# Performance work log

Hardware: AMD Instinct MI355X
Metric: run time of the kernel (lower is better)

Reference implementation:

```python
import jax, jax.numpy as jnp
import numpy as np

N_NODE, N_REL = 200000, 64
DIM, N_FACTOR, N_LAYER, K, B = 64, 4, 2, 32, 1024


def setup_inputs() -> dict:
    key = jax.random.key(0)
    ks = jax.random.split(key, 12)
    node_emb = jax.random.normal(ks[0], (N_NODE, N_FACTOR, DIM), jnp.float32) * 0.05
    relation_emb = jax.random.normal(ks[1], (N_REL, N_FACTOR, DIM), jnp.float32) * 0.05
    # attention MLP: Linear(2d -> d), ReLU, Linear(d -> 1); stored as [in, out]
    W1 = jax.random.normal(ks[2], (2 * DIM, DIM), jnp.float32) * (1.0 / np.sqrt(2 * DIM))
    b1 = jnp.zeros((DIM,), jnp.float32)
    W2 = jax.random.normal(ks[3], (DIM, 1), jnp.float32) * (1.0 / np.sqrt(DIM))
    b2 = jnp.zeros((1,), jnp.float32)
    users = jax.random.randint(ks[4], (B,), 0, N_NODE)
    items = jax.random.randint(ks[5], (B,), 0, N_NODE)

    def make_triple(kh, kr, kt):
        h = jax.random.randint(kh, (B, 1, N_LAYER, K), 0, N_NODE)
        r = jax.random.randint(kr, (B, 1, N_LAYER, K), 0, N_REL)
        t = jax.random.randint(kt, (B, 1, N_LAYER, K), 0, N_NODE)
        return jnp.concatenate([h, r, t], axis=1)  # [B, 3, L, K]

    users_triple = make_triple(ks[6], ks[7], ks[8])
    items_triple = make_triple(ks[9], ks[10], ks[11])
    return {
        "node_emb": node_emb, "relation_emb": relation_emb,
        "W1": W1, "b1": b1, "W2": W2, "b2": b2,
        "users": users, "items": items,
        "users_triple": users_triple, "items_triple": items_triple,
    }


def _knowledge_attention(h_emb, t_emb, W1, b1, W2, b2):
    # h_emb, t_emb: [B, L, K, F, d]
    x = jnp.concatenate([h_emb, t_emb], axis=-1)          # [B,L,K,F,2d]
    hid = jax.nn.relu(x @ W1 + b1)                        # [B,L,K,F,d]
    logits = jnp.squeeze(hid @ W2 + b2, axis=-1)          # [B,L,K,F]
    w = jax.nn.softmax(logits, axis=2)                    # softmax over neighbors K
    return jnp.sum(w[..., None] * t_emb, axis=2)          # [B,L,F,d]


def _tower(node_emb, idx, triple, W1, b1, W2, b2):
    origin = node_emb[idx]                                # [B,F,d]
    h = node_emb[triple[:, 0]]                            # [B,L,K,F,d]
    t = node_emb[triple[:, 2]]                            # [B,L,K,F,d]
    layers = _knowledge_attention(h, t, W1, b1, W2, b2)   # [B,L,F,d]
    emb = jnp.concatenate([origin[:, None], layers], axis=1)  # [B,L+1,F,d]
    return jnp.transpose(emb, (1, 0, 2, 3))               # [L+1,B,F,d]


def reference(node_emb, relation_emb, W1, b1, W2, b2, users, items, users_triple, items_triple):
    # relation_emb is gathered in the original but never used by the attention math.
    u = _tower(node_emb, users, users_triple, W1, b1, W2, b2)
    v = _tower(node_emb, items, items_triple, W1, b1, W2, b2)
    return jnp.stack([u, v])  # [2, L+1, B, F, d]
```

## Files before the change

### kernel.cpp

```cpp
#include <hip/hip_runtime.h>
#include <math.h>

#define NNODE  200000
#define DIM    64
#define NF     4
#define NLAYER 2
#define KK     32
#define BB     1024

typedef __bf16 bf16x8 __attribute__((ext_vector_type(8)));
typedef float  f32x4  __attribute__((ext_vector_type(4)));

__global__ void prep_w1t(const float* __restrict__ W1, __bf16* __restrict__ w1t) {
    int j = blockIdx.x * 256 + threadIdx.x;
    int d = j >> 7, i = j & 127;
    w1t[j] = (__bf16)W1[i * 64 + d];
}

__global__ __launch_bounds__(256, 3) void kgat_direct(
    const float* __restrict__ node_emb,
    const __bf16* __restrict__ w1t,
    const float* __restrict__ b1,
    const float* __restrict__ W2,
    const int*   __restrict__ users,
    const int*   __restrict__ items,
    const int*   __restrict__ users_triple,
    const int*   __restrict__ items_triple,
    float*       __restrict__ out)
{
    __shared__ float logitS[128];

    const int bid   = blockIdx.x;
    const int tower = bid >> 11;
    const int b     = (bid >> 1) & 1023;
    const int layer = bid & 1;
    const int tid   = threadIdx.x;
    const int w     = tid >> 6;
    const int lane  = tid & 63;
    const int m16   = lane & 15;
    const int quad  = lane >> 4;

    const int* __restrict__ triple = tower ? items_triple : users_triple;
    const int* __restrict__ idxarr = tower ? items : users;

    const int hbase = ((b * 3 + 0) * NLAYER + layer) * KK;
    const int tbase = ((b * 3 + 2) * NLAYER + layer) * KK;

    int hi[2], ti[2];
    hi[0] = triple[hbase + m16];
    hi[1] = triple[hbase + 16 + m16];
    ti[0] = triple[tbase + m16];
    ti[1] = triple[tbase + 16 + m16];
    const int tkv = triple[tbase + (lane & 31)];

    bf16x8 Af[2][4];
#pragma unroll
    for (int mt = 0; mt < 2; ++mt) {
        const float* __restrict__ rh = node_emb + ((size_t)hi[mt] * NF + w) * DIM;
        const float* __restrict__ rt = node_emb + ((size_t)ti[mt] * NF + w) * DIM;
#pragma unroll
        for (int kt = 0; kt < 4; ++kt) {
            const float* __restrict__ src = (kt < 2 ? rh : rt) + (kt & 1) * 32 + quad * 8;
            f32x4 v0 = *(const f32x4*)src;
            f32x4 v1 = *(const f32x4*)(src + 4);
            bf16x8 a;
#pragma unroll
            for (int u = 0; u < 4; ++u) { a[u] = (__bf16)v0[u]; a[4 + u] = (__bf16)v1[u]; }
            Af[mt][kt] = a;
        }
    }

    float tv[KK];
#pragma unroll
    for (int k = 0; k < KK; ++k) {
        const int tk = __shfl(tkv, k, 64);
        tv[k] = node_emb[((size_t)tk * NF + w) * DIM + lane];
    }

    f32x4 C[2][4];
#pragma unroll
    for (int mt = 0; mt < 2; ++mt)
#pragma unroll
        for (int nt = 0; nt < 4; ++nt) C[mt][nt] = (f32x4)(0.f);

#pragma unroll
    for (int kt = 0; kt < 4; ++kt) {
        bf16x8 Bn[4];
#pragma unroll
        for (int nt = 0; nt < 4; ++nt)
            Bn[nt] = *(const bf16x8*)(w1t + (nt * 16 + m16) * 128 + kt * 32 + quad * 8);
#pragma unroll
        for (int nt = 0; nt < 4; ++nt) {
            C[0][nt] = __builtin_amdgcn_mfma_f32_16x16x32_bf16(Af[0][kt], Bn[nt], C[0][nt], 0, 0, 0);
            C[1][nt] = __builtin_amdgcn_mfma_f32_16x16x32_bf16(Af[1][kt], Bn[nt], C[1][nt], 0, 0, 0);
        }
    }

    float b1v[4], w2v[4];
#pragma unroll
    for (int nt = 0; nt < 4; ++nt) {
        b1v[nt] = b1[nt * 16 + m16];
        w2v[nt] = W2[nt * 16 + m16];
    }
    float lsum[2][4];
#pragma unroll
    for (int mt = 0; mt < 2; ++mt)
#pragma unroll
        for (int r = 0; r < 4; ++r) {
            float s = 0.f;
#pragma unroll
            for (int nt = 0; nt < 4; ++nt)
                s += fmaxf(C[mt][nt][r] + b1v[nt], 0.f) * w2v[nt];
            lsum[mt][r] = s;
        }
#pragma unroll
    for (int off = 1; off < 16; off <<= 1)
#pragma unroll
        for (int mt = 0; mt < 2; ++mt)
#pragma unroll
            for (int r = 0; r < 4; ++r)
                lsum[mt][r] += __shfl_xor(lsum[mt][r], off, 64);

    if (m16 == 0) {
#pragma unroll
        for (int mt = 0; mt < 2; ++mt) {
            f32x4 v;
#pragma unroll
            for (int r = 0; r < 4; ++r) v[r] = lsum[mt][r];
            *(f32x4*)&logitS[w * 32 + mt * 16 + quad * 4] = v;
        }
    }
    const float lg = logitS[w * 32 + (lane & 31)];

    float mx = lg;
#pragma unroll
    for (int off = 16; off; off >>= 1) mx = fmaxf(mx, __shfl_xor(mx, off, 64));
    const float e = __expf(lg - mx);
    float s = e;
#pragma unroll
    for (int off = 16; off; off >>= 1) s += __shfl_xor(s, off, 64);
    const float wgt = e / s;

    float oacc = 0.f;
#pragma unroll
    for (int k = 0; k < KK; ++k)
        oacc += __shfl(wgt, k, 64) * tv[k];
    out[(((size_t)(tower * 3 + 1 + layer) * BB + b) * NF + w) * DIM + lane] = oacc;

    if (layer == 0) {
        const int oid = idxarr[b];
        out[(((size_t)(tower * 3 + 0) * BB + b) * NF + w) * DIM + lane] =
            node_emb[((size_t)oid * NF + w) * DIM + lane];
    }
}

extern "C" void kernel_launch(void* const* d_in, const int* in_sizes, int n_in,
                              void* d_out, int out_size, void* d_ws, size_t ws_size,
                              hipStream_t stream) {
    const float* node_emb     = (const float*)d_in[0];
    const float* W1           = (const float*)d_in[2];
    const float* b1           = (const float*)d_in[3];
    const float* W2           = (const float*)d_in[4];
    const float* b2           = (const float*)d_in[5]; (void)b2;
    const int*   users        = (const int*)d_in[6];
    const int*   items        = (const int*)d_in[7];
    const int*   users_triple = (const int*)d_in[8];
    const int*   items_triple = (const int*)d_in[9];
    float* out = (float*)d_out;

    __bf16* w1t = (__bf16*)d_ws;

    hipLaunchKernelGGL(prep_w1t, dim3(32), dim3(256), 0, stream, W1, w1t);
    hipLaunchKernelGGL(kgat_direct, dim3(2 * BB * NLAYER), dim3(256), 0, stream,
                       node_emb, w1t, b1, W2,
                       users, items, users_triple, items_triple, out);
}
```

Measured before the change: 322.7 us.

## Reuse bf16 tail fragments for weighted sum instead of re-gathering tail rows

The weighted neighbor sum now comes from the tail embeddings already loaded as bf16 MFMA A-fragments, so the second gather of 32 tail rows per wave is gone. Partial sums are reduced with cross-lane shuffles and staged through shared memory before a coalesced store. Dropping the 32-register tv array also allows raising the occupancy hint from 3 to 4 blocks per SM. The risk is lower precision, since the output is now built from bf16-rounded tail values, and more shuffle work in the reduction.

```diff
diff --git a/kernel.cpp b/kernel.cpp
--- a/kernel.cpp
+++ b/kernel.cpp
@@ -17,7 +17,7 @@
     w1t[j] = (__bf16)W1[i * 64 + d];
 }
 
-__global__ __launch_bounds__(256, 3) void kgat_direct(
+__global__ __launch_bounds__(256, 4) void kgat_direct(
     const float* __restrict__ node_emb,
     const __bf16* __restrict__ w1t,
     const float* __restrict__ b1,
@@ -29,6 +29,7 @@
     float*       __restrict__ out)
 {
     __shared__ float logitS[128];
+    __shared__ float outS[256];
 
     const int bid   = blockIdx.x;
     const int tower = bid >> 11;
@@ -51,7 +52,6 @@
     hi[1] = triple[hbase + 16 + m16];
     ti[0] = triple[tbase + m16];
     ti[1] = triple[tbase + 16 + m16];
-    const int tkv = triple[tbase + (lane & 31)];
 
     bf16x8 Af[2][4];
 #pragma unroll
@@ -70,13 +70,6 @@
         }
     }
 
-    float tv[KK];
-#pragma unroll
-    for (int k = 0; k < KK; ++k) {
-        const int tk = __shfl(tkv, k, 64);
-        tv[k] = node_emb[((size_t)tk * NF + w) * DIM + lane];
-    }
-
     f32x4 C[2][4];
 #pragma unroll
     for (int mt = 0; mt < 2; ++mt)
@@ -141,11 +134,42 @@
     for (int off = 16; off; off >>= 1) s += __shfl_xor(s, off, 64);
     const float wgt = e / s;
 
-    float oacc = 0.f;
-#pragma unroll
-    for (int k = 0; k < KK; ++k)
-        oacc += __shfl(wgt, k, 64) * tv[k];
-    out[(((size_t)(tower * 3 + 1 + layer) * BB + b) * NF + w) * DIM + lane] = oacc;
+    float o0[8], o1[8];
+#pragma unroll
+    for (int j = 0; j < 8; ++j) { o0[j] = 0.f; o1[j] = 0.f; }
+#pragma unroll
+    for (int mt = 0; mt < 2; ++mt) {
+        const float wv = __shfl(wgt, mt * 16 + m16, 64);
+#pragma unroll
+        for (int j = 0; j < 8; ++j) {
+            o0[j] += wv * (float)Af[mt][2][j];
+            o1[j] += wv * (float)Af[mt][3][j];
+        }
+    }
+#pragma unroll
+    for (int off = 1; off < 16; off <<= 1)
+#pragma unroll
+        for (int j = 0; j < 8; ++j) {
+            o0[j] += __shfl_xor(o0[j], off, 64);
+            o1[j] += __shfl_xor(o1[j], off, 64);
+        }
+    if (m16 == 0) {
+        f32x4 v;
+#pragma unroll
+        for (int j = 0; j < 4; ++j) v[j] = o0[j];
+        *(f32x4*)&outS[w * 64 + quad * 8] = v;
+#pragma unroll
+        for (int j = 0; j < 4; ++j) v[j] = o0[4 + j];
+        *(f32x4*)&outS[w * 64 + quad * 8 + 4] = v;
+#pragma unroll
+        for (int j = 0; j < 4; ++j) v[j] = o1[j];
+        *(f32x4*)&outS[w * 64 + 32 + quad * 8] = v;
+#pragma unroll
+        for (int j = 0; j < 4; ++j) v[j] = o1[4 + j];
+        *(f32x4*)&outS[w * 64 + 32 + quad * 8 + 4] = v;
+    }
+    out[(((size_t)(tower * 3 + 1 + layer) * BB + b) * NF + w) * DIM + lane] =
+        outS[w * 64 + lane];
 
     if (layer == 0) {
         const int oid = idxarr[b];
```

Result: faster. 304.0 us (-5.8%).
